# Optimization experiments

Measured on AMD Instinct MI355X. Metric: run time of the kernel, lower is better.

The kernel has to match this reference:

```python
import jax, jax.numpy as jnp
import numpy as np

LEAKY = 0.2     # PyG GATConv leaky_relu negative slope
BN_EPS = 1e-5

N, E, F_IN = 100000, 1600000, 7
ENC, HID, HEADS = 64, 32, 4
HC = HID * HEADS          # 128
DEC_IN, OUT = 64, 4
N_HIDDEN = 2              # nb_hidden_layers - 1


def gat_conv(z, src, dst, W, a_src, a_dst, b, concat):
    # PyG GATConv (shared lin for src/dst), dropout in eval mode = identity.
    n = z.shape[0]
    H, C = a_src.shape
    h = (z @ W).reshape(n, H, C)                      # [N,H,C]
    al_s = jnp.einsum('nhc,hc->nh', h, a_src)         # [N,H]
    al_d = jnp.einsum('nhc,hc->nh', h, a_dst)
    e = jax.nn.leaky_relu(al_s[src] + al_d[dst], LEAKY)   # [E,H]
    m = jax.ops.segment_max(e, dst, num_segments=n)       # scatter-softmax over in-edges
    ex = jnp.exp(e - m[dst])
    denom = jax.ops.segment_sum(ex, dst, num_segments=n)
    alpha = ex / (denom[dst] + 1e-16)                     # [E,H]
    out = jax.ops.segment_sum(h[src] * alpha[:, :, None], dst, num_segments=n)  # [N,H,C]
    out = out.reshape(n, H * C) if concat else out.mean(axis=1)
    return out + b


def batch_norm(z, gamma, beta):
    # track_running_stats=False -> always use batch statistics (biased var)
    mu = z.mean(axis=0)
    var = z.var(axis=0)
    return gamma * (z - mu) * jax.lax.rsqrt(var + BN_EPS) + beta


def setup_inputs() -> dict:
    key = jax.random.key(0)
    ks = jax.random.split(key, 20)
    g = lambda k, shape, fan: jax.random.normal(k, shape, jnp.float32) * (1.0 / np.sqrt(fan))
    inp = {
        'x': jax.random.normal(ks[0], (N, F_IN), jnp.float32),
        'edge_index': jax.random.randint(ks[1], (2, E), 0, N, jnp.int32),
        'enc_W': g(ks[2], (F_IN, ENC), F_IN),
        'enc_b': jnp.zeros((ENC,), jnp.float32),
        'in_W': g(ks[3], (ENC, HC), ENC),
        'in_att_src': g(ks[4], (HEADS, HID), HID),
        'in_att_dst': g(ks[5], (HEADS, HID), HID),
        'in_b': jnp.zeros((HC,), jnp.float32),
        'hid_W': g(ks[6], (N_HIDDEN, HC, HC), HC),
        'hid_att_src': g(ks[7], (N_HIDDEN, HEADS, HID), HID),
        'hid_att_dst': g(ks[8], (N_HIDDEN, HEADS, HID), HID),
        'hid_b': jnp.zeros((N_HIDDEN, HC), jnp.float32),
        'bn_gamma': jnp.ones((1 + N_HIDDEN, HC), jnp.float32),
        'bn_beta': jnp.zeros((1 + N_HIDDEN, HC), jnp.float32),
        'out_W': g(ks[9], (HC, DEC_IN), HC),           # out heads=1, concat=False
        'out_att_src': g(ks[10], (1, DEC_IN), DEC_IN),
        'out_att_dst': g(ks[11], (1, DEC_IN), DEC_IN),
        'out_b': jnp.zeros((DEC_IN,), jnp.float32),
        'dec_W': g(ks[12], (DEC_IN, OUT), DEC_IN),
        'dec_b': jnp.zeros((OUT,), jnp.float32),
    }
    return inp


def reference(x, edge_index, enc_W, enc_b, in_W, in_att_src, in_att_dst, in_b,
              hid_W, hid_att_src, hid_att_dst, hid_b, bn_gamma, bn_beta,
              out_W, out_att_src, out_att_dst, out_b, dec_W, dec_b):
    n = x.shape[0]
    loops = jnp.arange(n, dtype=edge_index.dtype)      # PyG GATConv add_self_loops=True
    src = jnp.concatenate([edge_index[0], loops])
    dst = jnp.concatenate([edge_index[1], loops])

    z = x @ enc_W + enc_b                              # encoder
    z = gat_conv(z, src, dst, in_W, in_att_src, in_att_dst, in_b, concat=True)
    z = jax.nn.relu(batch_norm(z, bn_gamma[0], bn_beta[0]))
    for i in range(N_HIDDEN):
        z = gat_conv(z, src, dst, hid_W[i], hid_att_src[i], hid_att_dst[i], hid_b[i], concat=True)
        z = jax.nn.relu(batch_norm(z, bn_gamma[i + 1], bn_beta[i + 1]))
    z = gat_conv(z, src, dst, out_W, out_att_src, out_att_dst, out_b, concat=False)
    z = z @ dec_W + dec_b                              # decoder
    return z
```

## Files before the change

### kernel.cpp

```cpp
#include <hip/hip_runtime.h>
#include <math.h>

#define LEAKY 0.2f
#define BN_EPS 1e-5f

typedef unsigned short u16;
typedef __bf16 bf16x8 __attribute__((ext_vector_type(8)));
typedef float f32x4 __attribute__((ext_vector_type(4)));
typedef u16 ushort8 __attribute__((ext_vector_type(8)));

__device__ __forceinline__ u16 f2bf(float x){
    unsigned u = __float_as_uint(x);
    u += 0x7FFFu + ((u >> 16) & 1u);
    return (u16)(u >> 16);
}
__device__ __forceinline__ float bf2f(u16 b){ return __uint_as_float(((unsigned)b) << 16); }


__global__ __launch_bounds__(256) void k_encoder(const float* __restrict__ x,
        const float* __restrict__ W, const float* __restrict__ b,
        float* __restrict__ z, int N){
    int gid = blockIdx.x*256 + threadIdx.x;
    int n = gid >> 6, j = gid & 63;
    if (n >= N) return;
    float acc = b[j];
    #pragma unroll
    for (int k=0;k<7;k++) acc += x[n*7+k]*W[k*64+j];
    z[(size_t)n*64+j] = acc;
}

template<int K, int M>
__global__ __launch_bounds__(256) void k_pack_w(const float* __restrict__ W,
        u16* __restrict__ hi, u16* __restrict__ lo){
    int idx = blockIdx.x*256 + threadIdx.x;
    if (idx >= K*M) return;
    int e = idx & 7, l16 = (idx >> 3) & 3, rest = idx >> 5;
    int n = rest % M, t = rest / M;
    int k = t*32 + l16*8 + e;
    float w = W[(size_t)k*M + n];
    u16 hb = f2bf(w);
    hi[idx] = hb;
    lo[idx] = f2bf(w - bf2f(hb));
}

__global__ void k_bn_coef(const float* __restrict__ cs, const float* __restrict__ cq,
        const float* __restrict__ g, const float* __restrict__ be,
        float* __restrict__ scale, float* __restrict__ shift, float invN){
    int j = threadIdx.x;
    float mu = cs[j]*invN;
    float var = cq[j]*invN - mu*mu;
    float s = g[j]*rsqrtf(var + BN_EPS);
    scale[j] = s; shift[j] = be[j] - mu*s;
}


template<int H>
__global__ __launch_bounds__(256) void k_mh1(const float* __restrict__ al,
        float* __restrict__ pm, int total){
    int t = threadIdx.x;
    float m = -1e30f;
    for (int i = blockIdx.x*256 + t; i < total; i += 64*256)
        m = fmaxf(m, al[i]);
    #pragma unroll
    for (int off = H; off < 64; off <<= 1)
        m = fmaxf(m, __shfl_xor(m, off, 64));
    __shared__ float ws[16];
    int lane = t & 63, wid = t >> 6;
    if (lane < H) ws[wid*H + lane] = m;
    __syncthreads();
    if (t < H){
        float mm = ws[t];
        #pragma unroll
        for (int w = 1; w < 4; w++) mm = fmaxf(mm, ws[w*H + t]);
        pm[blockIdx.x*H + t] = mm;
    }
}

template<int H>
__global__ void k_mh2(const float* __restrict__ pm, float* __restrict__ mh){
    int t = threadIdx.x;
    float m = -1e30f;
    #pragma unroll
    for (int k = 0; k < H; k++) m = fmaxf(m, pm[t + k*64]);
    #pragma unroll
    for (int off = H; off < 64; off <<= 1)
        m = fmaxf(m, __shfl_xor(m, off, 64));
    if (t < H) mh[t] = m;
}

template<int K, int M, int RW, int CW, int WR, int WC, int H, bool BNIN>
__global__ __launch_bounds__(256) void k_gemm(const float* __restrict__ z,
        const u16* __restrict__ Whi, const u16* __restrict__ Wlo,
        const float* __restrict__ bnscale, const float* __restrict__ bnshift,
        const float* __restrict__ a_src, const float* __restrict__ a_dst,
        u16* __restrict__ hout, float* __restrict__ al_s, float* __restrict__ al_d,
        int N)
{
    static_assert(RW*CW == 4 && RW*WR*16 == 64 && CW*WC*16 == M, "tile config");
    constexpr int KS = K/32;
    constexpr int KG = K/8;
    __shared__ __align__(16) u16 Ahi[64*K];
    __shared__ __align__(16) u16 Alo[64*K];
    const int brow = blockIdx.x*64;
    const int tid = threadIdx.x;

    for (int u = tid; u < 64*KG; u += 256){
        int row = u / KG, kg = u % KG;
        int gr = brow + row;
        float v[8];
        if (gr < N){
            const float4* p = (const float4*)(z + (size_t)gr*K + kg*8);
            float4 a = p[0], bq = p[1];
            v[0]=a.x; v[1]=a.y; v[2]=a.z; v[3]=a.w;
            v[4]=bq.x; v[5]=bq.y; v[6]=bq.z; v[7]=bq.w;
            if (BNIN){
                const float4* sc = (const float4*)(bnscale + kg*8);
                const float4* sh = (const float4*)(bnshift + kg*8);
                float4 s0=sc[0], s1=sc[1], t0=sh[0], t1=sh[1];
                v[0]=fmaxf(fmaf(v[0],s0.x,t0.x),0.f);
                v[1]=fmaxf(fmaf(v[1],s0.y,t0.y),0.f);
                v[2]=fmaxf(fmaf(v[2],s0.z,t0.z),0.f);
                v[3]=fmaxf(fmaf(v[3],s0.w,t0.w),0.f);
                v[4]=fmaxf(fmaf(v[4],s1.x,t1.x),0.f);
                v[5]=fmaxf(fmaf(v[5],s1.y,t1.y),0.f);
                v[6]=fmaxf(fmaf(v[6],s1.z,t1.z),0.f);
                v[7]=fmaxf(fmaf(v[7],s1.w,t1.w),0.f);
            }
        } else {
            #pragma unroll
            for (int e=0;e<8;e++) v[e]=0.f;
        }
        ushort8 h8, l8;
        #pragma unroll
        for (int e=0;e<8;e++){
            u16 hb = f2bf(v[e]);
            h8[e] = hb;
            l8[e] = f2bf(v[e] - bf2f(hb));
        }
        int rb = row >> 4, t = kg >> 2, lg = kg & 3;
        int base = (((rb*KS + t)*64) + (row & 15) + 16*lg)*8;
        *(ushort8*)&Ahi[base] = h8;
        *(ushort8*)&Alo[base] = l8;
    }
    __syncthreads();

    const int wave = tid >> 6, lane = tid & 63;
    const int wrow = wave / CW, wcol = wave % CW;
    const int l15 = lane & 15, l16 = lane >> 4;

    f32x4 acc[WR][WC];
    #pragma unroll
    for (int r=0;r<WR;r++)
        #pragma unroll
        for (int c=0;c<WC;c++) acc[r][c] = (f32x4){0.f,0.f,0.f,0.f};

    #pragma unroll
    for (int t = 0; t < KS; ++t){
        bf16x8 ah[WR], al[WR];
        #pragma unroll
        for (int r=0;r<WR;r++){
            int rb = wrow*WR + r;
            int off = ((rb*KS + t)*64 + lane)*8;
            ah[r] = *(const bf16x8*)&Ahi[off];
            al[r] = *(const bf16x8*)&Alo[off];
        }
        bf16x8 bh[WC], bl[WC];
        #pragma unroll
        for (int c=0;c<WC;c++){
            int n = (wcol*WC + c)*16 + l15;
            size_t off = ((size_t)(t*M + n)*4 + (size_t)l16)*8;
            bh[c] = *(const bf16x8*)&Whi[off];
            bl[c] = *(const bf16x8*)&Wlo[off];
        }
        #pragma unroll
        for (int r=0;r<WR;r++)
            #pragma unroll
            for (int c=0;c<WC;c++){
                acc[r][c] = __builtin_amdgcn_mfma_f32_16x16x32_bf16(al[r], bh[c], acc[r][c], 0,0,0);
                acc[r][c] = __builtin_amdgcn_mfma_f32_16x16x32_bf16(ah[r], bl[c], acc[r][c], 0,0,0);
                acc[r][c] = __builtin_amdgcn_mfma_f32_16x16x32_bf16(ah[r], bh[c], acc[r][c], 0,0,0);
            }
    }

    float as_[WC], ad_[WC];
    #pragma unroll
    for (int c=0;c<WC;c++){
        int colg = (wcol*WC + c)*16 + l15;
        as_[c] = a_src[colg]; ad_[c] = a_dst[colg];
    }
    #pragma unroll
    for (int r=0;r<WR;r++){
        #pragma unroll
        for (int q=0;q<4;q++){
            int rowg = brow + (wrow*WR + r)*16 + l16*4 + q;
            float s0=0.f,d0=0.f,s1=0.f,d1=0.f;
            #pragma unroll
            for (int c=0;c<WC;c++){
                float av = acc[r][c][q];
                if (H==1 || c < WC/2){ s0 += av*as_[c]; d0 += av*ad_[c]; }
                else                 { s1 += av*as_[c]; d1 += av*ad_[c]; }
            }
            #pragma unroll
            for (int off=1; off<16; off<<=1){
                s0 += __shfl_xor(s0, off, 64); d0 += __shfl_xor(d0, off, 64);
                if (H==4){ s1 += __shfl_xor(s1, off, 64); d1 += __shfl_xor(d1, off, 64); }
            }
            if (l15 == 0 && rowg < N){
                if (H==4){
                    al_s[(size_t)rowg*4 + wcol*2]     = s0;
                    al_s[(size_t)rowg*4 + wcol*2 + 1] = s1;
                    al_d[(size_t)rowg*4 + wcol*2]     = d0;
                    al_d[(size_t)rowg*4 + wcol*2 + 1] = d1;
                } else {
                    al_s[rowg] = s0; al_d[rowg] = d0;
                }
            }
        }
    }

    #pragma unroll
    for (int r=0;r<WR;r++)
        #pragma unroll
        for (int c=0;c<WC;c++){
            int colg = (wcol*WC + c)*16 + l15;
            #pragma unroll
            for (int q=0;q<4;q++){
                int rowg = brow + (wrow*WR + r)*16 + l16*4 + q;
                if (rowg < N) hout[(size_t)rowg*M + colg] = f2bf(acc[r][c][q]);
            }
        }
}


__global__ __launch_bounds__(256) void k_deg(const int* __restrict__ ei, int E,
        int* __restrict__ deg){
    int e = blockIdx.x*256 + threadIdx.x;
    if (e < E) atomicAdd(deg + ei[E+e], 1);
}

__device__ __forceinline__ int wave_scan(int v, int lane){
    #pragma unroll
    for (int off=1; off<64; off<<=1){
        int t = __shfl_up(v, off, 64);
        if (lane >= off) v += t;
    }
    return v;
}

__global__ __launch_bounds__(1024) void k_scan1(const int* __restrict__ deg,
        int* __restrict__ excl, int* __restrict__ bsum, int N){
    __shared__ int ws[16];
    int i = blockIdx.x*1024 + threadIdx.x;
    int lane = threadIdx.x & 63, wid = threadIdx.x >> 6;
    int v = (i < N) ? deg[i] : 0;
    int inc = wave_scan(v, lane);
    if (lane == 63) ws[wid] = inc;
    __syncthreads();
    if (wid == 0){
        int wv = (lane < 16) ? ws[lane] : 0;
        int winc = wave_scan(wv, lane);
        if (lane < 16) ws[lane] = winc - wv;
    }
    __syncthreads();
    int off = ws[wid];
    if (i < N) excl[i] = off + inc - v;
    if (threadIdx.x == 1023) bsum[blockIdx.x] = off + inc;
}

__global__ void k_scan2(int* __restrict__ bsum, int nb){
    if (threadIdx.x == 0 && blockIdx.x == 0){
        int c = 0;
        for (int i = 0; i < nb; i++){ int t = bsum[i]; bsum[i] = c; c += t; }
    }
}

__global__ __launch_bounds__(256) void k_scan3(const int* __restrict__ excl,
        const int* __restrict__ bsum, int* __restrict__ rowptr,
        int* __restrict__ cursor, int N, int E){
    int i = blockIdx.x*256 + threadIdx.x;
    if (i < N){
        int r = excl[i] + bsum[i >> 10];
        rowptr[i] = r; cursor[i] = r;
    } else if (i == N){
        rowptr[N] = E;
    }
}

__global__ __launch_bounds__(256) void k_bucket(const int* __restrict__ ei, int E,
        int* __restrict__ cursor, int* __restrict__ csr){
    int e = blockIdx.x*256 + threadIdx.x;
    if (e >= E) return;
    int pos = atomicAdd(cursor + ei[E+e], 1);
    csr[pos] = ei[e];
}


template<int H, int C, bool STATS, bool DECODE>
__global__ __launch_bounds__(256) void k_gat_agg(
        const int* __restrict__ rowptr, const int* __restrict__ csr_src,
        const float* __restrict__ al_s, const float* __restrict__ al_d,
        const float* __restrict__ mh,
        const u16* __restrict__ hfeat, const float* __restrict__ b,
        float* __restrict__ z, float* __restrict__ cs, float* __restrict__ cq,
        const float* __restrict__ decW, const float* __restrict__ decb,
        float* __restrict__ out, int N, int totWaves)
{
    constexpr int M = H*C;
    constexpr int GS = M/8;
    constexpr int EPS = 64/GS;
    const int lane = threadIdx.x & 63;
    const int q = lane % GS;
    const int g = lane / GS;
    const int col0 = q*8;
    const int hd = col0 / C;
    const int gw = blockIdx.x*4 + (threadIdx.x >> 6);

    const float mhf = mh[hd];
    float bj[8];
    #pragma unroll
    for (int j=0;j<8;j++) bj[j] = b[col0+j];

    float w[8][4];
    if (DECODE){
        #pragma unroll
        for (int j=0;j<8;j++)
            #pragma unroll
            for (int o=0;o<4;o++) w[j][o] = decW[(col0+j)*4 + o];
    }
    float ls[8], lq[8];
    if (STATS){
        #pragma unroll
        for (int j=0;j<8;j++){ ls[j]=0.f; lq[j]=0.f; }
    }

    for (int dst = gw; dst < N; dst += totWaves){
        int p0 = rowptr[dst], p1 = rowptr[dst+1];
        float ald = al_d[(size_t)dst*H + hd];
        float v0 = al_s[(size_t)dst*H + hd] + ald;
        v0 = v0 > 0.f ? v0 : LEAKY*v0;
        float tt = mhf + ald;
        float mb = tt > 0.f ? tt : LEAKY*tt;
        mb = fminf(mb, v0 + 40.f);

        float ex0 = __expf(v0 - mb) * (1.0f/EPS);
        float s = ex0;
        float acc[8];
        ushort8 hd8 = *(const ushort8*)(hfeat + (size_t)dst*M + col0);
        #pragma unroll
        for (int j=0;j<8;j++) acc[j] = bf2f(hd8[j]) * ex0;

        auto LD = [&](int base, ushort8& hv, float& vs){
            int idx = base + g;
            int src = dst;
            if (idx < p1) src = csr_src[idx];
            float t = al_s[(size_t)src*H + hd];
            vs = (idx < p1) ? t : -1e30f;
            hv = *(const ushort8*)(hfeat + (size_t)src*M + col0);
        };
        auto PR = [&](const ushort8& hv, float vs){
            float vv = vs + ald;
            vv = vv > 0.f ? vv : LEAKY*vv;
            float ex = __expf(vv - mb);
            s += ex;
            #pragma unroll
            for (int j=0;j<8;j++) acc[j] = fmaf(bf2f(hv[j]), ex, acc[j]);
        };

        ushort8 hvA, hvB; float vsA=0.f, vsB=0.f;
        int p = p0;
        LD(p, hvA, vsA);
        while (p < p1){
            LD(p+EPS, hvB, vsB);
            PR(hvA, vsA);
            p += EPS;
            if (p >= p1) break;
            LD(p+EPS, hvA, vsA);
            PR(hvB, vsB);
            p += EPS;
        }

        #pragma unroll
        for (int off = GS; off < 64; off <<= 1){
            s += __shfl_xor(s, off, 64);
            #pragma unroll
            for (int j=0;j<8;j++) acc[j] += __shfl_xor(acc[j], off, 64);
        }
        float inv = 1.f/s;
        float o8[8];
        #pragma unroll
        for (int j=0;j<8;j++) o8[j] = acc[j]*inv + bj[j];

        if (STATS){
            #pragma unroll
            for (int j=0;j<8;j++){ ls[j] += o8[j]; lq[j] += o8[j]*o8[j]; }
        }
        if (!DECODE){
            if (lane < GS){
                f32x4 w0v = {o8[0],o8[1],o8[2],o8[3]};
                f32x4 w1v = {o8[4],o8[5],o8[6],o8[7]};
                __builtin_nontemporal_store(w0v, (f32x4*)(z + (size_t)dst*M + col0));
                __builtin_nontemporal_store(w1v, (f32x4*)(z + (size_t)dst*M + col0 + 4));
            }
        } else {
            float p4[4] = {0.f,0.f,0.f,0.f};
            #pragma unroll
            for (int j=0;j<8;j++)
                #pragma unroll
                for (int o=0;o<4;o++) p4[o] = fmaf(o8[j], w[j][o], p4[o]);
            #pragma unroll
            for (int off=1; off<GS; off<<=1){
                #pragma unroll
                for (int o=0;o<4;o++) p4[o] += __shfl_xor(p4[o], off, 64);
            }
            if (lane == 0){
                f32x4 o = {p4[0]+decb[0], p4[1]+decb[1], p4[2]+decb[2], p4[3]+decb[3]};
                __builtin_nontemporal_store(o, (f32x4*)(out + (size_t)dst*4));
            }
        }
    }

    if (STATS){
        __shared__ float sls[128], slq[128];
        if (threadIdx.x < 128){ sls[threadIdx.x]=0.f; slq[threadIdx.x]=0.f; }
        __syncthreads();
        if (lane < GS){
            #pragma unroll
            for (int j=0;j<8;j++){
                atomicAdd(&sls[col0+j], ls[j]);
                atomicAdd(&slq[col0+j], lq[j]);
            }
        }
        __syncthreads();
        if (threadIdx.x < 128){
            atomicAdd(cs + threadIdx.x, sls[threadIdx.x]);
            atomicAdd(cq + threadIdx.x, slq[threadIdx.x]);
        }
    }
}

extern "C" void kernel_launch(void* const* d_in, const int* in_sizes, int n_in,
                              void* d_out, int out_size, void* d_ws, size_t ws_size,
                              hipStream_t stream){
    const float* x      = (const float*)d_in[0];
    const int*   ei     = (const int*)  d_in[1];
    const float* enc_W  = (const float*)d_in[2];
    const float* enc_b  = (const float*)d_in[3];
    const float* in_W   = (const float*)d_in[4];
    const float* in_as  = (const float*)d_in[5];
    const float* in_ad  = (const float*)d_in[6];
    const float* in_b   = (const float*)d_in[7];
    const float* hid_W  = (const float*)d_in[8];
    const float* hid_as = (const float*)d_in[9];
    const float* hid_ad = (const float*)d_in[10];
    const float* hid_b  = (const float*)d_in[11];
    const float* bn_g   = (const float*)d_in[12];
    const float* bn_b   = (const float*)d_in[13];
    const float* out_W  = (const float*)d_in[14];
    const float* out_as = (const float*)d_in[15];
    const float* out_ad = (const float*)d_in[16];
    const float* out_b  = (const float*)d_in[17];
    const float* dec_W  = (const float*)d_in[18];
    const float* dec_b  = (const float*)d_in[19];

    const int N = in_sizes[0] / 7;
    const int E = in_sizes[1] / 2;
    const int NB = (N + 1023) / 1024;
    const int NT = (N + 63) / 64;
    const int AGG_BLOCKS = 2048, TOT_WAVES = AGG_BLOCKS*4;

    float*    bufZ   = (float*)d_ws;
    float*    al_s   = bufZ + (size_t)N*128;
    float*    al_d   = al_s + (size_t)N*4;
    float*    cs     = al_d + (size_t)N*4;
    float*    cq     = cs + 128;
    float*    mh     = cq + 128;
    float*    pm     = mh + 8;
    float*    scale  = pm + 256;
    float*    shift  = scale + 128;
    int*      deg    = (int*)(shift + 128);
    int*      excl   = deg + N;
    int*      rowptr = excl + N;
    int*      cursor = rowptr + (N+1);
    int*      bsum   = cursor + N;
    int*      csr    = bsum + NB;
    u16*      hb     = (u16*)(((uintptr_t)(csr + E) + 15) & ~(uintptr_t)15);
    u16*      wk     = hb + (size_t)N*128;
    u16* wk_in_hi  = wk;                    u16* wk_in_lo  = wk_in_hi  + 64*128;
    u16* wk_h0_hi  = wk_in_lo  + 64*128;    u16* wk_h0_lo  = wk_h0_hi  + 128*128;
    u16* wk_h1_hi  = wk_h0_lo  + 128*128;   u16* wk_h1_lo  = wk_h1_hi  + 128*128;
    u16* wk_out_hi = wk_h1_lo  + 128*128;   u16* wk_out_lo = wk_out_hi + 128*64;

    k_pack_w<64,128><<<(64*128+255)/256, 256, 0, stream>>>(in_W, wk_in_hi, wk_in_lo);
    k_pack_w<128,128><<<(128*128+255)/256, 256, 0, stream>>>(hid_W, wk_h0_hi, wk_h0_lo);
    k_pack_w<128,128><<<(128*128+255)/256, 256, 0, stream>>>(hid_W + 128*128, wk_h1_hi, wk_h1_lo);
    k_pack_w<128,64><<<(128*64+255)/256, 256, 0, stream>>>(out_W, wk_out_hi, wk_out_lo);

    hipMemsetAsync(deg, 0, (size_t)N*sizeof(int), stream);
    k_deg   <<<(E+255)/256, 256, 0, stream>>>(ei, E, deg);
    k_scan1 <<<NB, 1024, 0, stream>>>(deg, excl, bsum, N);
    k_scan2 <<<1, 64, 0, stream>>>(bsum, NB);
    k_scan3 <<<(N+1+255)/256, 256, 0, stream>>>(excl, bsum, rowptr, cursor, N, E);
    k_bucket<<<(E+255)/256, 256, 0, stream>>>(ei, E, cursor, csr);

    k_encoder<<<(N*64+255)/256, 256, 0, stream>>>(x, enc_W, enc_b, bufZ, N);

    const float invN = 1.f/(float)N;

    hipMemsetAsync(cs, 0, 256*sizeof(float), stream);
    k_gemm<64,128,2,2,2,4,4,false><<<NT, 256, 0, stream>>>(bufZ, wk_in_hi, wk_in_lo,
            nullptr, nullptr, in_as, in_ad, hb, al_s, al_d, N);
    k_mh1<4><<<64, 256, 0, stream>>>(al_s, pm, N*4);
    k_mh2<4><<<1, 64, 0, stream>>>(pm, mh);
    k_gat_agg<4,32,true,false><<<AGG_BLOCKS, 256, 0, stream>>>(rowptr, csr, al_s, al_d, mh,
            hb, in_b, bufZ, cs, cq, nullptr, nullptr, nullptr, N, TOT_WAVES);
    k_bn_coef<<<1, 128, 0, stream>>>(cs, cq, bn_g, bn_b, scale, shift, invN);

    for (int i = 0; i < 2; i++){
        const u16* whi = i ? wk_h1_hi : wk_h0_hi;
        const u16* wlo = i ? wk_h1_lo : wk_h0_lo;
        hipMemsetAsync(cs, 0, 256*sizeof(float), stream);
        k_gemm<128,128,2,2,2,4,4,true><<<NT, 256, 0, stream>>>(bufZ, whi, wlo,
                scale, shift, hid_as + (size_t)i*128, hid_ad + (size_t)i*128,
                hb, al_s, al_d, N);
        k_mh1<4><<<64, 256, 0, stream>>>(al_s, pm, N*4);
        k_mh2<4><<<1, 64, 0, stream>>>(pm, mh);
        k_gat_agg<4,32,true,false><<<AGG_BLOCKS, 256, 0, stream>>>(rowptr, csr, al_s, al_d, mh,
                hb, hid_b + (size_t)i*128, bufZ, cs, cq, nullptr, nullptr, nullptr, N, TOT_WAVES);
        k_bn_coef<<<1, 128, 0, stream>>>(cs, cq, bn_g + (i+1)*128, bn_b + (i+1)*128, scale, shift, invN);
    }

    k_gemm<128,64,4,1,1,4,1,true><<<NT, 256, 0, stream>>>(bufZ, wk_out_hi, wk_out_lo,
            scale, shift, out_as, out_ad, hb, al_s, al_d, N);
    k_mh1<1><<<64, 256, 0, stream>>>(al_s, pm, N);
    k_mh2<1><<<1, 64, 0, stream>>>(pm, mh);
    k_gat_agg<1,64,false,true><<<AGG_BLOCKS, 256, 0, stream>>>(rowptr, csr, al_s, al_d, mh,
            hb, out_b, nullptr, nullptr, nullptr, dec_W, dec_b, (float*)d_out, N, TOT_WAVES);
}
```

Before: 938.5 us.

## Fold attention vectors into extra GEMM columns and swizzle LDS A layout

Precomputes W·a_src and W·a_dst per head as 16 extra packed weight columns, so the GEMM produces the attention logits directly through additional MFMA tiles instead of a per-row dot-product and shuffle-reduction epilogue. Only the wcol==0 waves compute the extra tile, which adds some imbalance across waves. It also XOR-swizzles the shared-memory A tile layout to reduce LDS bank conflicts. Precision changes slightly because the logits are now computed from split-bf16 products of the folded vectors rather than from the fp32 accumulators.

```diff
diff --git a/kernel.cpp b/kernel.cpp
--- a/kernel.cpp
+++ b/kernel.cpp
@@ -29,18 +29,41 @@
     z[(size_t)n*64+j] = acc;
 }
 
-template<int K, int M>
+template<int K, int MW, int MT>
 __global__ __launch_bounds__(256) void k_pack_w(const float* __restrict__ W,
         u16* __restrict__ hi, u16* __restrict__ lo){
     int idx = blockIdx.x*256 + threadIdx.x;
-    if (idx >= K*M) return;
+    if (idx >= K*MW) return;
     int e = idx & 7, l16 = (idx >> 3) & 3, rest = idx >> 5;
-    int n = rest % M, t = rest / M;
+    int n = rest % MW, t = rest / MW;
     int k = t*32 + l16*8 + e;
-    float w = W[(size_t)k*M + n];
+    float w = W[(size_t)k*MW + n];
     u16 hb = f2bf(w);
-    hi[idx] = hb;
-    lo[idx] = f2bf(w - bf2f(hb));
+    size_t o = ((size_t)(t*MT + n)*4 + (size_t)l16)*8 + e;
+    hi[o] = hb;
+    lo[o] = f2bf(w - bf2f(hb));
+}
+
+template<int K, int MW, int MT, int H, int C>
+__global__ __launch_bounds__(256) void k_pack_a(const float* __restrict__ W,
+        const float* __restrict__ as, const float* __restrict__ ad,
+        u16* __restrict__ hi, u16* __restrict__ lo){
+    int idx = blockIdx.x*256 + threadIdx.x;
+    if (idx >= K*16) return;
+    int e = idx & 7, l16 = (idx >> 3) & 3, rest = idx >> 5;
+    int j = rest % 16, t = rest / 16;
+    int k = t*32 + l16*8 + e;
+    float v = 0.f;
+    if (j < 2*H){
+        int hh = j >> 1;
+        const float* a = (j & 1) ? ad : as;
+        for (int c = 0; c < C; c++)
+            v += W[(size_t)k*MW + hh*C + c] * a[hh*C + c];
+    }
+    u16 hb = f2bf(v);
+    size_t o = ((size_t)(t*MT + MW + j)*4 + (size_t)l16)*8 + e;
+    hi[o] = hb;
+    lo[o] = f2bf(v - bf2f(hb));
 }
 
 __global__ void k_bn_coef(const float* __restrict__ cs, const float* __restrict__ cq,
@@ -88,15 +111,15 @@
     if (t < H) mh[t] = m;
 }
 
-template<int K, int M, int RW, int CW, int WR, int WC, int H, bool BNIN>
+template<int K, int MW, int RW, int CW, int WR, int WC, int H, bool BNIN>
 __global__ __launch_bounds__(256) void k_gemm(const float* __restrict__ z,
         const u16* __restrict__ Whi, const u16* __restrict__ Wlo,
         const float* __restrict__ bnscale, const float* __restrict__ bnshift,
-        const float* __restrict__ a_src, const float* __restrict__ a_dst,
         u16* __restrict__ hout, float* __restrict__ al_s, float* __restrict__ al_d,
         int N)
 {
-    static_assert(RW*CW == 4 && RW*WR*16 == 64 && CW*WC*16 == M, "tile config");
+    static_assert(RW*CW == 4 && RW*WR*16 == 64 && CW*WC*16 == MW, "tile config");
+    constexpr int MT = MW + 16;
     constexpr int KS = K/32;
     constexpr int KG = K/8;
     __shared__ __align__(16) u16 Ahi[64*K];
@@ -138,9 +161,10 @@
             l8[e] = f2bf(v[e] - bf2f(hb));
         }
         int rb = row >> 4, t = kg >> 2, lg = kg & 3;
-        int base = (((rb*KS + t)*64) + (row & 15) + 16*lg)*8;
-        *(ushort8*)&Ahi[base] = h8;
-        *(ushort8*)&Alo[base] = l8;
+        int gidx = (rb*KS + t)*64 + (row & 15) + 16*lg;
+        gidx ^= (gidx >> 4) & 7;
+        *(ushort8*)&Ahi[gidx*8] = h8;
+        *(ushort8*)&Alo[gidx*8] = l8;
     }
     __syncthreads();
 
@@ -149,10 +173,13 @@
     const int l15 = lane & 15, l16 = lane >> 4;
 
     f32x4 acc[WR][WC];
-    #pragma unroll
-    for (int r=0;r<WR;r++)
+    f32x4 acc_e[WR];
+    #pragma unroll
+    for (int r=0;r<WR;r++){
+        acc_e[r] = (f32x4){0.f,0.f,0.f,0.f};
         #pragma unroll
         for (int c=0;c<WC;c++) acc[r][c] = (f32x4){0.f,0.f,0.f,0.f};
+    }
 
     #pragma unroll
     for (int t = 0; t < KS; ++t){
@@ -160,15 +187,16 @@
         #pragma unroll
         for (int r=0;r<WR;r++){
             int rb = wrow*WR + r;
-            int off = ((rb*KS + t)*64 + lane)*8;
-            ah[r] = *(const bf16x8*)&Ahi[off];
-            al[r] = *(const bf16x8*)&Alo[off];
+            int goff = (rb*KS + t)*64 + lane;
+            goff ^= (goff >> 4) & 7;
+            ah[r] = *(const bf16x8*)&Ahi[goff*8];
+            al[r] = *(const bf16x8*)&Alo[goff*8];
         }
         bf16x8 bh[WC], bl[WC];
         #pragma unroll
         for (int c=0;c<WC;c++){
             int n = (wcol*WC + c)*16 + l15;
-            size_t off = ((size_t)(t*M + n)*4 + (size_t)l16)*8;
+            size_t off = ((size_t)(t*MT + n)*4 + (size_t)l16)*8;
             bh[c] = *(const bf16x8*)&Whi[off];
             bl[c] = *(const bf16x8*)&Wlo[off];
         }
@@ -180,42 +208,37 @@
                 acc[r][c] = __builtin_amdgcn_mfma_f32_16x16x32_bf16(ah[r], bl[c], acc[r][c], 0,0,0);
                 acc[r][c] = __builtin_amdgcn_mfma_f32_16x16x32_bf16(ah[r], bh[c], acc[r][c], 0,0,0);
             }
-    }
-
-    float as_[WC], ad_[WC];
-    #pragma unroll
-    for (int c=0;c<WC;c++){
-        int colg = (wcol*WC + c)*16 + l15;
-        as_[c] = a_src[colg]; ad_[c] = a_dst[colg];
-    }
-    #pragma unroll
-    for (int r=0;r<WR;r++){
-        #pragma unroll
-        for (int q=0;q<4;q++){
-            int rowg = brow + (wrow*WR + r)*16 + l16*4 + q;
-            float s0=0.f,d0=0.f,s1=0.f,d1=0.f;
-            #pragma unroll
-            for (int c=0;c<WC;c++){
-                float av = acc[r][c][q];
-                if (H==1 || c < WC/2){ s0 += av*as_[c]; d0 += av*ad_[c]; }
-                else                 { s1 += av*as_[c]; d1 += av*ad_[c]; }
-            }
-            #pragma unroll
-            for (int off=1; off<16; off<<=1){
-                s0 += __shfl_xor(s0, off, 64); d0 += __shfl_xor(d0, off, 64);
-                if (H==4){ s1 += __shfl_xor(s1, off, 64); d1 += __shfl_xor(d1, off, 64); }
-            }
-            if (l15 == 0 && rowg < N){
-                if (H==4){
-                    al_s[(size_t)rowg*4 + wcol*2]     = s0;
-                    al_s[(size_t)rowg*4 + wcol*2 + 1] = s1;
-                    al_d[(size_t)rowg*4 + wcol*2]     = d0;
-                    al_d[(size_t)rowg*4 + wcol*2 + 1] = d1;
-                } else {
-                    al_s[rowg] = s0; al_d[rowg] = d0;
+        if (wcol == 0){
+            size_t offE = ((size_t)(t*MT + MW + l15)*4 + (size_t)l16)*8;
+            bf16x8 bhe = *(const bf16x8*)&Whi[offE];
+            bf16x8 ble = *(const bf16x8*)&Wlo[offE];
+            #pragma unroll
+            for (int r=0;r<WR;r++){
+                acc_e[r] = __builtin_amdgcn_mfma_f32_16x16x32_bf16(al[r], bhe, acc_e[r], 0,0,0);
+                acc_e[r] = __builtin_amdgcn_mfma_f32_16x16x32_bf16(ah[r], ble, acc_e[r], 0,0,0);
+                acc_e[r] = __builtin_amdgcn_mfma_f32_16x16x32_bf16(ah[r], bhe, acc_e[r], 0,0,0);
+            }
+        }
+    }
+
+    if (wcol == 0 && l15 < 2*H){
+        int j = l15;
+        #pragma unroll
+        for (int r=0;r<WR;r++)
+            #pragma unroll
+            for (int q=0;q<4;q++){
+                int rowg = brow + (wrow*WR + r)*16 + l16*4 + q;
+                if (rowg < N){
+                    float v = acc_e[r][q];
+                    if (H==4){
+                        if (j & 1) al_d[(size_t)rowg*4 + (j>>1)] = v;
+                        else       al_s[(size_t)rowg*4 + (j>>1)] = v;
+                    } else {
+                        if (j & 1) al_d[rowg] = v;
+                        else       al_s[rowg] = v;
+                    }
                 }
             }
-        }
     }
 
     #pragma unroll
@@ -226,7 +249,7 @@
             #pragma unroll
             for (int q=0;q<4;q++){
                 int rowg = brow + (wrow*WR + r)*16 + l16*4 + q;
-                if (rowg < N) hout[(size_t)rowg*M + colg] = f2bf(acc[r][c][q]);
+                if (rowg < N) hout[(size_t)rowg*MW + colg] = f2bf(acc[r][c][q]);
             }
         }
 }
@@ -485,15 +508,19 @@
     int*      csr    = bsum + NB;
     u16*      hb     = (u16*)(((uintptr_t)(csr + E) + 15) & ~(uintptr_t)15);
     u16*      wk     = hb + (size_t)N*128;
-    u16* wk_in_hi  = wk;                    u16* wk_in_lo  = wk_in_hi  + 64*128;
-    u16* wk_h0_hi  = wk_in_lo  + 64*128;    u16* wk_h0_lo  = wk_h0_hi  + 128*128;
-    u16* wk_h1_hi  = wk_h0_lo  + 128*128;   u16* wk_h1_lo  = wk_h1_hi  + 128*128;
-    u16* wk_out_hi = wk_h1_lo  + 128*128;   u16* wk_out_lo = wk_out_hi + 128*64;
-
-    k_pack_w<64,128><<<(64*128+255)/256, 256, 0, stream>>>(in_W, wk_in_hi, wk_in_lo);
-    k_pack_w<128,128><<<(128*128+255)/256, 256, 0, stream>>>(hid_W, wk_h0_hi, wk_h0_lo);
-    k_pack_w<128,128><<<(128*128+255)/256, 256, 0, stream>>>(hid_W + 128*128, wk_h1_hi, wk_h1_lo);
-    k_pack_w<128,64><<<(128*64+255)/256, 256, 0, stream>>>(out_W, wk_out_hi, wk_out_lo);
+    u16* wk_in_hi  = wk;                     u16* wk_in_lo  = wk_in_hi  + 64*144;
+    u16* wk_h0_hi  = wk_in_lo  + 64*144;     u16* wk_h0_lo  = wk_h0_hi  + 128*144;
+    u16* wk_h1_hi  = wk_h0_lo  + 128*144;    u16* wk_h1_lo  = wk_h1_hi  + 128*144;
+    u16* wk_out_hi = wk_h1_lo  + 128*144;    u16* wk_out_lo = wk_out_hi + 128*80;
+
+    k_pack_w<64,128,144><<<(64*128+255)/256, 256, 0, stream>>>(in_W, wk_in_hi, wk_in_lo);
+    k_pack_a<64,128,144,4,32><<<(64*16+255)/256, 256, 0, stream>>>(in_W, in_as, in_ad, wk_in_hi, wk_in_lo);
+    k_pack_w<128,128,144><<<(128*128+255)/256, 256, 0, stream>>>(hid_W, wk_h0_hi, wk_h0_lo);
+    k_pack_a<128,128,144,4,32><<<(128*16+255)/256, 256, 0, stream>>>(hid_W, hid_as, hid_ad, wk_h0_hi, wk_h0_lo);
+    k_pack_w<128,128,144><<<(128*128+255)/256, 256, 0, stream>>>(hid_W + 128*128, wk_h1_hi, wk_h1_lo);
+    k_pack_a<128,128,144,4,32><<<(128*16+255)/256, 256, 0, stream>>>(hid_W + 128*128, hid_as + 128, hid_ad + 128, wk_h1_hi, wk_h1_lo);
+    k_pack_w<128,64,80><<<(128*64+255)/256, 256, 0, stream>>>(out_W, wk_out_hi, wk_out_lo);
+    k_pack_a<128,64,80,1,64><<<(128*16+255)/256, 256, 0, stream>>>(out_W, out_as, out_ad, wk_out_hi, wk_out_lo);
 
     hipMemsetAsync(deg, 0, (size_t)N*sizeof(int), stream);
     k_deg   <<<(E+255)/256, 256, 0, stream>>>(ei, E, deg);
@@ -508,7 +535,7 @@
 
     hipMemsetAsync(cs, 0, 256*sizeof(float), stream);
     k_gemm<64,128,2,2,2,4,4,false><<<NT, 256, 0, stream>>>(bufZ, wk_in_hi, wk_in_lo,
-            nullptr, nullptr, in_as, in_ad, hb, al_s, al_d, N);
+            nullptr, nullptr, hb, al_s, al_d, N);
     k_mh1<4><<<64, 256, 0, stream>>>(al_s, pm, N*4);
     k_mh2<4><<<1, 64, 0, stream>>>(pm, mh);
     k_gat_agg<4,32,true,false><<<AGG_BLOCKS, 256, 0, stream>>>(rowptr, csr, al_s, al_d, mh,
@@ -520,8 +547,7 @@
         const u16* wlo = i ? wk_h1_lo : wk_h0_lo;
         hipMemsetAsync(cs, 0, 256*sizeof(float), stream);
         k_gemm<128,128,2,2,2,4,4,true><<<NT, 256, 0, stream>>>(bufZ, whi, wlo,
-                scale, shift, hid_as + (size_t)i*128, hid_ad + (size_t)i*128,
-                hb, al_s, al_d, N);
+                scale, shift, hb, al_s, al_d, N);
         k_mh1<4><<<64, 256, 0, stream>>>(al_s, pm, N*4);
         k_mh2<4><<<1, 64, 0, stream>>>(pm, mh);
         k_gat_agg<4,32,true,false><<<AGG_BLOCKS, 256, 0, stream>>>(rowptr, csr, al_s, al_d, mh,
@@ -530,7 +556,7 @@
     }
 
     k_gemm<128,64,4,1,1,4,1,true><<<NT, 256, 0, stream>>>(bufZ, wk_out_hi, wk_out_lo,
-            scale, shift, out_as, out_ad, hb, al_s, al_d, N);
+            scale, shift, hb, al_s, al_d, N);
     k_mh1<1><<<64, 256, 0, stream>>>(al_s, pm, N);
     k_mh2<1><<<1, 64, 0, stream>>>(pm, mh);
     k_gat_agg<1,64,false,true><<<AGG_BLOCKS, 256, 0, stream>>>(rowptr, csr, al_s, al_d, mh,
```

New measurement: 944.6 us. About the same (+0.6%).
